# Performance work log

Hardware: AMD Instinct MI355X
Metric: run time of the kernel (lower is better)

The kernel has to match this reference:

```python
import jax, jax.numpy as jnp
import numpy as np

N = 50000   # nodes
D = 128     # hidden_dim
H = 8       # num_heads
DK = D // H # per-head dim
E = 1600000 # edges
L = 2       # n_layers
LN_EPS = 1e-5


def _layer_norm(x, g, b):
    m = jnp.mean(x, axis=-1, keepdims=True)
    v = jnp.mean(jnp.square(x - m), axis=-1, keepdims=True)
    return (x - m) * jax.lax.rsqrt(v + LN_EPS) * g + b


def _gt_layer(h, src, dst, Wq, bq, Wk, bk, Wv, bv, Wo, bo, W1, b1, W2, b2, g1, be1, g2, be2):
    n = h.shape[0]
    Q = (h @ Wq + bq).reshape(n, H, DK)
    K = (h @ Wk + bk).reshape(n, H, DK)
    V = (h @ Wv + bv).reshape(n, H, DK)
    # per-edge scaled dot-product score: K[src] . Q[dst]
    score = jnp.einsum('ehd,ehd->eh', K[src], Q[dst]) / np.sqrt(DK)
    score = jnp.exp(jnp.clip(score, -5.0, 5.0))            # [E,H]
    wV = jax.ops.segment_sum(V[src] * score[:, :, None], dst, num_segments=n)  # [N,H,DK]
    z = jax.ops.segment_sum(score, dst, num_segments=n)    # [N,H]
    attn = wV / (z[:, :, None] + 1e-6)                     # possible_empty-safe softmax
    h_att = attn.reshape(n, D) @ Wo + bo
    h = _layer_norm(h + h_att, g1, be1)                    # residual + LN
    ffn = jax.nn.relu(h @ W1 + b1) @ W2 + b2
    h = _layer_norm(h + ffn, g2, be2)                      # residual + LN
    return h


def setup_inputs() -> dict:
    key = jax.random.key(0)
    ks = jax.random.split(key, 16)
    s = 1.0 / np.sqrt(D)
    s2 = 1.0 / np.sqrt(2 * D)
    w = lambda k, shape, sc: jax.random.normal(k, shape, jnp.float32) * sc
    return {
        'h':   jax.random.normal(ks[0], (N, D), jnp.float32),
        'src': jax.random.randint(ks[1], (E,), 0, N),
        'dst': jax.random.randint(ks[2], (E,), 0, N),
        'Wq': w(ks[3], (L, D, D), s), 'bq': jnp.zeros((L, D), jnp.float32),
        'Wk': w(ks[4], (L, D, D), s), 'bk': jnp.zeros((L, D), jnp.float32),
        'Wv': w(ks[5], (L, D, D), s), 'bv': jnp.zeros((L, D), jnp.float32),
        'Wo': w(ks[6], (L, D, D), s), 'bo': jnp.zeros((L, D), jnp.float32),
        'W1': w(ks[7], (L, D, 2 * D), s), 'b1': jnp.zeros((L, 2 * D), jnp.float32),
        'W2': w(ks[8], (L, 2 * D, D), s2), 'b2': jnp.zeros((L, D), jnp.float32),
        'ln1_g': jnp.ones((L, D), jnp.float32), 'ln1_b': jnp.zeros((L, D), jnp.float32),
        'ln2_g': jnp.ones((L, D), jnp.float32), 'ln2_b': jnp.zeros((L, D), jnp.float32),
    }


def reference(h, src, dst, Wq, bq, Wk, bk, Wv, bv, Wo, bo, W1, b1, W2, b2, ln1_g, ln1_b, ln2_g, ln2_b):
    for l in range(L):
        h = _gt_layer(h, src, dst, Wq[l], bq[l], Wk[l], bk[l], Wv[l], bv[l],
                      Wo[l], bo[l], W1[l], b1[l], W2[l], b2[l],
                      ln1_g[l], ln1_b[l], ln2_g[l], ln2_b[l])
    return h
```

## Files before the change

kernel.cpp:

```cpp
#include <hip/hip_runtime.h>

#define NN 50000
#define DD 128
#define HH 8
#define EE 1600000
#define LL 2

typedef unsigned short u16;
typedef __attribute__((ext_vector_type(8))) __bf16 bf16x8;
typedef __attribute__((ext_vector_type(4))) float f32x4;
typedef __attribute__((ext_vector_type(2))) float f32x2;

__device__ __forceinline__ float bf2f(u16 u){
    return __uint_as_float(((unsigned int)u) << 16);
}
__device__ __forceinline__ u16 f2bf(float f){
    unsigned int x = __float_as_uint(f);
    x = x + 0x7fff + ((x >> 16) & 1);
    return (u16)(x >> 16);
}

__global__ __launch_bounds__(256) void f2b4_kernel(const float* __restrict__ in, u16* __restrict__ out, int n4){
    int i = blockIdx.x * 256 + threadIdx.x;
    if (i < n4){
        float4 v = ((const float4*)in)[i];
        ushort4 o;
        o.x = f2bf(v.x); o.y = f2bf(v.y); o.z = f2bf(v.z); o.w = f2bf(v.w);
        ((ushort4*)out)[i] = o;
    }
}

#define FILL_SUB 128
__global__ __launch_bounds__(256) void count_kernel(const int* __restrict__ dst, int* __restrict__ cnt){
    int slice = blockIdx.x & 7;
    int sub = blockIdx.x >> 3;
    int lo = slice * (NN / 8), hi = lo + (NN / 8);
    for (int e = sub * 256 + threadIdx.x; e < EE; e += FILL_SUB * 256){
        int d = dst[e];
        if (d >= lo && d < hi) atomicAdd(&cnt[d], 1);
    }
}

__global__ __launch_bounds__(1024) void scan_kernel(const int* __restrict__ cnt,
                                                    int* __restrict__ offs, int* __restrict__ cur){
    __shared__ int wsum[16];
    __shared__ int carry_s;
    __shared__ int ctot_s;
    int t = threadIdx.x, lane = t & 63, w = t >> 6;
    if (t == 0){ offs[0] = 0; cur[0] = 0; carry_s = 0; }
    __syncthreads();
    const int N4 = NN / 4;
    for (int base = 0; base < N4; base += 1024){
        int i4 = base + t;
        int4 x = (i4 < N4) ? ((const int4*)cnt)[i4] : make_int4(0, 0, 0, 0);
        int s1 = x.x, s2 = s1 + x.y, s3 = s2 + x.z, s4 = s3 + x.w;
        int v = s4;
        #pragma unroll
        for (int d = 1; d < 64; d <<= 1){ int u = __shfl_up(v, d); if (lane >= d) v += u; }
        if (lane == 63) wsum[w] = v;
        __syncthreads();
        if (t < 16){
            int sv = wsum[t];
            int iv = sv;
            #pragma unroll
            for (int d = 1; d < 16; d <<= 1){ int u = __shfl_up(iv, d); if (t >= d) iv += u; }
            wsum[t] = iv - sv;
            if (t == 15) ctot_s = iv;
        }
        __syncthreads();
        int excl = carry_s + wsum[w] + (v - s4);
        if (i4 < N4){
            int o = 4 * i4;
            offs[o + 1] = excl + s1;  cur[o + 1] = excl + s1;
            offs[o + 2] = excl + s2;  cur[o + 2] = excl + s2;
            offs[o + 3] = excl + s3;  cur[o + 3] = excl + s3;
            offs[o + 4] = excl + s4;  cur[o + 4] = excl + s4;
        }
        __syncthreads();
        if (t == 0) carry_s += ctot_s;
        __syncthreads();
    }
}

__global__ __launch_bounds__(256) void fill_kernel(const int* __restrict__ src, const int* __restrict__ dst,
                                                   int* __restrict__ cur, int* __restrict__ srcs){
    int slice = blockIdx.x & 7;
    int sub = blockIdx.x >> 3;
    int lo = slice * (NN / 8), hi = lo + (NN / 8);
    for (int e = sub * 256 + threadIdx.x; e < EE; e += FILL_SUB * 256){
        int d = dst[e];
        if (d >= lo && d < hi){
            int p = atomicAdd(&cur[d], 1);
            srcs[p] = src[e];
        }
    }
}

__global__ __launch_bounds__(256) void qkvpack_kernel(const float* __restrict__ Wq, const float* __restrict__ Wk,
                                                      const float* __restrict__ Wv, const float* __restrict__ bq,
                                                      const float* __restrict__ bk, const float* __restrict__ bv,
                                                      u16* __restrict__ Wt, float* __restrict__ bcat){
    int l = blockIdx.y;
    int idx = blockIdx.x * 256 + threadIdx.x;
    if (idx < 384 * 128){
        int n = idx >> 7, k = idx & 127;
        const float* W = (n < 128) ? Wq : (n < 256) ? Wk : Wv;
        int nc = n & 127;
        Wt[(size_t)l * 384 * 128 + idx] = f2bf(W[(size_t)l * 128 * 128 + k * 128 + nc]);
        if (k == 0){
            const float* bb = (n < 128) ? bq : (n < 256) ? bk : bv;
            bcat[l * 384 + n] = bb[l * 128 + nc];
        }
    }
}

__global__ __launch_bounds__(256) void transpose_kernel(const float* __restrict__ in, u16* __restrict__ out,
                                                        int R, int C){
    size_t mat = (size_t)blockIdx.y * R * C;
    int idx = blockIdx.x * 256 + threadIdx.x;
    if (idx < R * C){
        int r = idx / C, c = idx % C;
        out[mat + (size_t)c * R + r] = f2bf(in[mat + idx]);
    }
}

#define BM 128
#define BKK 64
#define LDA 72
#define LDC 136

__global__ __launch_bounds__(256) void gemm_bf16(const u16* __restrict__ A, const u16* __restrict__ Wt,
                                                 const float* __restrict__ bias,
                                                 u16* __restrict__ out, int M, int K, int N, int relu){
    __shared__ __align__(16) char smem[128 * LDA * 2 * 2];
    u16* As = (u16*)smem;
    u16* Bs = As + 128 * LDA;
    u16* Cs = (u16*)smem;

    int tid = threadIdx.x;
    int m0 = blockIdx.x * BM, n0 = blockIdx.y * 128;
    int lane = tid & 63, w = tid >> 6;
    int wm = w >> 1, wn = w & 1;
    int l15 = lane & 15, hi = lane >> 4, lk = hi * 8;

    f32x4 acc[4][4];
    #pragma unroll
    for (int mi = 0; mi < 4; mi++)
        #pragma unroll
        for (int ni = 0; ni < 4; ni++)
            acc[mi][ni] = (f32x4){0.f, 0.f, 0.f, 0.f};

    int sr = tid >> 3;
    int sc = (tid & 7) * 8;

    for (int k0 = 0; k0 < K; k0 += BKK){
        __syncthreads();
        #pragma unroll
        for (int p = 0; p < 4; p++){
            int row = p * 32 + sr;
            int gm = m0 + row;
            uint4 va = make_uint4(0, 0, 0, 0);
            if (gm < M) va = *(const uint4*)(A + (size_t)gm * K + k0 + sc);
            *(uint4*)(&As[row * LDA + sc]) = va;
            uint4 vb = *(const uint4*)(Wt + (size_t)(n0 + row) * K + k0 + sc);
            *(uint4*)(&Bs[row * LDA + sc]) = vb;
        }
        __syncthreads();
        #pragma unroll
        for (int ks = 0; ks < 2; ks++){
            bf16x8 a[4], b[4];
            #pragma unroll
            for (int i = 0; i < 4; i++){
                a[i] = *(const bf16x8*)(&As[(wm * 64 + i * 16 + l15) * LDA + ks * 32 + lk]);
                b[i] = *(const bf16x8*)(&Bs[(wn * 64 + i * 16 + l15) * LDA + ks * 32 + lk]);
            }
            #pragma unroll
            for (int mi = 0; mi < 4; mi++)
                #pragma unroll
                for (int ni = 0; ni < 4; ni++)
                    acc[mi][ni] = __builtin_amdgcn_mfma_f32_16x16x32_bf16(a[mi], b[ni], acc[mi][ni], 0, 0, 0);
        }
    }

    __syncthreads();
    #pragma unroll
    for (int mi = 0; mi < 4; mi++)
        #pragma unroll
        for (int ni = 0; ni < 4; ni++){
            int col = wn * 64 + ni * 16 + l15;
            float bval = bias[n0 + col];
            #pragma unroll
            for (int j = 0; j < 4; j++){
                int rl = wm * 64 + mi * 16 + hi * 4 + j;
                float v = acc[mi][ni][j] + bval;
                if (relu) v = fmaxf(v, 0.f);
                Cs[rl * LDC + col] = f2bf(v);
            }
        }
    __syncthreads();
    int qrow = tid >> 4, quad = tid & 15;
    #pragma unroll
    for (int p = 0; p < 8; p++){
        int rl = p * 16 + qrow;
        int gr = m0 + rl;
        if (gr < M){
            uint4 v = *(const uint4*)(&Cs[rl * LDC + quad * 8]);
            *(uint4*)(out + (size_t)gr * N + n0 + quad * 8) = v;
        }
    }
}

__global__ __launch_bounds__(256) void gemm_qkv(const u16* __restrict__ A, const u16* __restrict__ Wt,
                                                const float* __restrict__ bias,
                                                u16* __restrict__ Qb, u16* __restrict__ Kb,
                                                unsigned char* __restrict__ Vb,
                                                int M, int K){
    __shared__ __align__(16) char smem[128 * LDA * 2 * 2];
    u16* As = (u16*)smem;
    u16* Bs = As + 128 * LDA;
    u16* Cs = (u16*)smem;

    int tid = threadIdx.x;
    int m0 = blockIdx.x * BM, n0 = blockIdx.y * 128;
    int lane = tid & 63, w = tid >> 6;
    int wm = w >> 1, wn = w & 1;
    int l15 = lane & 15, hi = lane >> 4, lk = hi * 8;

    f32x4 acc[4][4];
    #pragma unroll
    for (int mi = 0; mi < 4; mi++)
        #pragma unroll
        for (int ni = 0; ni < 4; ni++)
            acc[mi][ni] = (f32x4){0.f, 0.f, 0.f, 0.f};

    int sr = tid >> 3;
    int sc = (tid & 7) * 8;

    for (int k0 = 0; k0 < K; k0 += BKK){
        __syncthreads();
        #pragma unroll
        for (int p = 0; p < 4; p++){
            int row = p * 32 + sr;
            int gm = m0 + row;
            uint4 va = make_uint4(0, 0, 0, 0);
            if (gm < M) va = *(const uint4*)(A + (size_t)gm * K + k0 + sc);
            *(uint4*)(&As[row * LDA + sc]) = va;
            uint4 vb = *(const uint4*)(Wt + (size_t)(n0 + row) * K + k0 + sc);
            *(uint4*)(&Bs[row * LDA + sc]) = vb;
        }
        __syncthreads();
        #pragma unroll
        for (int ks = 0; ks < 2; ks++){
            bf16x8 a[4], b[4];
            #pragma unroll
            for (int i = 0; i < 4; i++){
                a[i] = *(const bf16x8*)(&As[(wm * 64 + i * 16 + l15) * LDA + ks * 32 + lk]);
                b[i] = *(const bf16x8*)(&Bs[(wn * 64 + i * 16 + l15) * LDA + ks * 32 + lk]);
            }
            #pragma unroll
            for (int mi = 0; mi < 4; mi++)
                #pragma unroll
                for (int ni = 0; ni < 4; ni++)
                    acc[mi][ni] = __builtin_amdgcn_mfma_f32_16x16x32_bf16(a[mi], b[ni], acc[mi][ni], 0, 0, 0);
        }
    }

    __syncthreads();
    #pragma unroll
    for (int mi = 0; mi < 4; mi++)
        #pragma unroll
        for (int ni = 0; ni < 4; ni++){
            int col = wn * 64 + ni * 16 + l15;
            float bval = bias[n0 + col];
            #pragma unroll
            for (int j = 0; j < 4; j++){
                int rl = wm * 64 + mi * 16 + hi * 4 + j;
                Cs[rl * LDC + col] = f2bf(acc[mi][ni][j] + bval);
            }
        }
    __syncthreads();
    int qrow = tid >> 4, quad = tid & 15;
    if (n0 < 256){
        u16* Tb = (n0 == 0) ? Qb : Kb;
        #pragma unroll
        for (int p = 0; p < 8; p++){
            int rl = p * 16 + qrow;
            int gr = m0 + rl;
            if (gr < M){
                uint4 v = *(const uint4*)(&Cs[rl * LDC + quad * 8]);
                *(uint4*)(Tb + (size_t)gr * 128 + quad * 8) = v;
            }
        }
    } else {
        #pragma unroll
        for (int p = 0; p < 8; p++){
            int rl = p * 16 + qrow;
            int gr = m0 + rl;
            if (gr < M){
                uint4 v = *(const uint4*)(&Cs[rl * LDC + quad * 8]);
                float f0 = bf2f((u16)(v.x & 0xffff)), f1 = bf2f((u16)(v.x >> 16));
                float f2 = bf2f((u16)(v.y & 0xffff)), f3 = bf2f((u16)(v.y >> 16));
                float f4 = bf2f((u16)(v.z & 0xffff)), f5 = bf2f((u16)(v.z >> 16));
                float f6 = bf2f((u16)(v.w & 0xffff)), f7 = bf2f((u16)(v.w >> 16));
                unsigned int w0 = __builtin_amdgcn_cvt_pk_fp8_f32(f0, f1, 0u, false);
                w0 = __builtin_amdgcn_cvt_pk_fp8_f32(f2, f3, w0, true);
                unsigned int w1 = __builtin_amdgcn_cvt_pk_fp8_f32(f4, f5, 0u, false);
                w1 = __builtin_amdgcn_cvt_pk_fp8_f32(f6, f7, w1, true);
                *(uint2*)(Vb + (size_t)gr * 128 + quad * 8) = make_uint2(w0, w1);
            }
        }
    }
}

__global__ __launch_bounds__(256) void gemm_ln(const u16* __restrict__ A, const u16* __restrict__ Wt,
                                               const float* __restrict__ bias, const u16* __restrict__ resid,
                                               const float* __restrict__ g, const float* __restrict__ b,
                                               u16* __restrict__ out_bf, float* __restrict__ out_f,
                                               int M, int K){
    __shared__ __align__(16) char smem[128 * LDA * 2 * 2];
    u16* As = (u16*)smem;
    u16* Bs = As + 128 * LDA;
    __shared__ float ps[2][128];
    __shared__ float pss[2][128];

    int tid = threadIdx.x;
    int m0 = blockIdx.x * BM;
    int lane = tid & 63, w = tid >> 6;
    int wm = w >> 1, wn = w & 1;
    int l15 = lane & 15, hi = lane >> 4, lk = hi * 8;

    f32x4 acc[4][4];
    #pragma unroll
    for (int mi = 0; mi < 4; mi++)
        #pragma unroll
        for (int ni = 0; ni < 4; ni++)
            acc[mi][ni] = (f32x4){0.f, 0.f, 0.f, 0.f};

    int sr = tid >> 3;
    int sc = (tid & 7) * 8;

    for (int k0 = 0; k0 < K; k0 += BKK){
        __syncthreads();
        #pragma unroll
        for (int p = 0; p < 4; p++){
            int row = p * 32 + sr;
            int gm = m0 + row;
            uint4 va = make_uint4(0, 0, 0, 0);
            if (gm < M) va = *(const uint4*)(A + (size_t)gm * K + k0 + sc);
            *(uint4*)(&As[row * LDA + sc]) = va;
            uint4 vb = *(const uint4*)(Wt + (size_t)row * K + k0 + sc);
            *(uint4*)(&Bs[row * LDA + sc]) = vb;
        }
        __syncthreads();
        #pragma unroll
        for (int ks = 0; ks < 2; ks++){
            bf16x8 a[4], bb[4];
            #pragma unroll
            for (int i = 0; i < 4; i++){
                a[i] = *(const bf16x8*)(&As[(wm * 64 + i * 16 + l15) * LDA + ks * 32 + lk]);
                bb[i] = *(const bf16x8*)(&Bs[(wn * 64 + i * 16 + l15) * LDA + ks * 32 + lk]);
            }
            #pragma unroll
            for (int mi = 0; mi < 4; mi++)
                #pragma unroll
                for (int ni = 0; ni < 4; ni++)
                    acc[mi][ni] = __builtin_amdgcn_mfma_f32_16x16x32_bf16(a[mi], bb[ni], acc[mi][ni], 0, 0, 0);
        }
    }

    float gcol[4], bcol[4], bval[4];
    #pragma unroll
    for (int ni = 0; ni < 4; ni++){
        int col = wn * 64 + ni * 16 + l15;
        gcol[ni] = g[col]; bcol[ni] = b[col]; bval[ni] = bias[col];
    }

    #pragma unroll
    for (int mi = 0; mi < 4; mi++)
        #pragma unroll
        for (int j = 0; j < 4; j++){
            int rl = wm * 64 + mi * 16 + hi * 4 + j;
            int gr = m0 + rl;
            float s = 0.f, ss = 0.f;
            #pragma unroll
            for (int ni = 0; ni < 4; ni++){
                int col = wn * 64 + ni * 16 + l15;
                float x = acc[mi][ni][j] + bval[ni];
                if (gr < M) x += bf2f(resid[(size_t)gr * 128 + col]);
                acc[mi][ni][j] = x;
                s += x; ss += x * x;
            }
            #pragma unroll
            for (int d = 1; d < 16; d <<= 1){
                s  += __shfl_xor(s, d);
                ss += __shfl_xor(ss, d);
            }
            if (l15 == 0){ ps[wn][rl] = s; pss[wn][rl] = ss; }
        }
    __syncthreads();

    #pragma unroll
    for (int mi = 0; mi < 4; mi++)
        #pragma unroll
        for (int j = 0; j < 4; j++){
            int rl = wm * 64 + mi * 16 + hi * 4 + j;
            int gr = m0 + rl;
            if (gr >= M) continue;
            float s = ps[0][rl] + ps[1][rl];
            float ss = pss[0][rl] + pss[1][rl];
            float mean = s * (1.f / 128.f);
            float var = ss * (1.f / 128.f) - mean * mean;
            float r = rsqrtf(var + 1e-5f);
            #pragma unroll
            for (int ni = 0; ni < 4; ni++){
                int col = wn * 64 + ni * 16 + l15;
                float o = (acc[mi][ni][j] - mean) * r * gcol[ni] + bcol[ni];
                if (out_f) out_f[(size_t)gr * 128 + col] = o;
                else       out_bf[(size_t)gr * 128 + col] = f2bf(o);
            }
        }
}

__global__ __launch_bounds__(256) void edge_attn_kernel(const u16* __restrict__ Qb,
                                                        const u16* __restrict__ Kb,
                                                        const unsigned char* __restrict__ Vb,
                                                        const int* __restrict__ srcs,
                                                        const int* __restrict__ offs,
                                                        u16* __restrict__ att){
    int n = blockIdx.x * 4 + (threadIdx.x >> 6);
    if (n >= NN) return;
    int lane = threadIdx.x & 63;
    int laneh = lane & 31;
    int half = lane >> 5;

    float q0, q1, q2, q3;
    {
        uint2 qv = *(const uint2*)(Qb + (size_t)n * 128 + 4 * laneh);
        q0 = bf2f((u16)(qv.x & 0xffff)); q1 = bf2f((u16)(qv.x >> 16));
        q2 = bf2f((u16)(qv.y & 0xffff)); q3 = bf2f((u16)(qv.y >> 16));
    }
    const u16* kbase = Kb + 4 * laneh;
    const unsigned char* vbase = Vb + 4 * laneh;

    float w0 = 0.f, w1 = 0.f, w2 = 0.f, w3 = 0.f, z = 0.f;
    const float CS = 0.25f * 1.44269504f;

    auto proc = [&](uint2 kk, unsigned int vv, float gate){
        float k0 = bf2f((u16)(kk.x & 0xffff)), k1 = bf2f((u16)(kk.x >> 16));
        float k2 = bf2f((u16)(kk.y & 0xffff)), k3 = bf2f((u16)(kk.y >> 16));
        float p = q0 * k0 + q1 * k1 + q2 * k2 + q3 * k3;
        p += __shfl_xor(p, 1);
        p += __shfl_xor(p, 2);
        p = fminf(fmaxf(p, -20.f), 20.f);
        float sc = __builtin_amdgcn_exp2f(p * CS) * gate;
        f32x2 vl = __builtin_amdgcn_cvt_pk_f32_fp8(vv, false);
        f32x2 vh = __builtin_amdgcn_cvt_pk_f32_fp8(vv, true);
        w0 += sc * vl[0]; w1 += sc * vl[1]; w2 += sc * vh[0]; w3 += sc * vh[1];
        z += sc;
    };

    int e0 = offs[n], e1 = offs[n + 1];
    int i = e0;
    for (; i + 15 < e1; i += 16){
        int s[8];
        #pragma unroll
        for (int u = 0; u < 8; u++) s[u] = srcs[i + 2 * u + half];
        uint2 kk[8];
        unsigned int vv[8];
        #pragma unroll
        for (int u = 0; u < 8; u++){
            kk[u] = *(const uint2*)(kbase + (size_t)s[u] * 128);
            vv[u] = *(const unsigned int*)(vbase + (size_t)s[u] * 128);
        }
        #pragma unroll
        for (int u = 0; u < 8; u++) proc(kk[u], vv[u], 1.f);
    }
    for (; i + 1 < e1; i += 2){
        int s = srcs[i + half];
        proc(*(const uint2*)(kbase + (size_t)s * 128),
             *(const unsigned int*)(vbase + (size_t)s * 128), 1.f);
    }
    if (i < e1){
        int s = srcs[i];
        proc(*(const uint2*)(kbase + (size_t)s * 128),
             *(const unsigned int*)(vbase + (size_t)s * 128), half ? 0.f : 1.f);
    }

    w0 += __shfl_xor(w0, 32); w1 += __shfl_xor(w1, 32);
    w2 += __shfl_xor(w2, 32); w3 += __shfl_xor(w3, 32);
    z  += __shfl_xor(z, 32);

    if (!half){
        float inv = 1.f / (z + 1e-6f);
        unsigned int oA = (unsigned int)f2bf(w0 * inv) | ((unsigned int)f2bf(w1 * inv) << 16);
        unsigned int oB = (unsigned int)f2bf(w2 * inv) | ((unsigned int)f2bf(w3 * inv) << 16);
        *(uint2*)(att + (size_t)n * DD + 4 * laneh) = make_uint2(oA, oB);
    }
}

extern "C" void kernel_launch(void* const* d_in, const int* in_sizes, int n_in,
                              void* d_out, int out_size, void* d_ws, size_t ws_size,
                              hipStream_t stream){
    const float* h_in = (const float*)d_in[0];
    const int* src  = (const int*)d_in[1];
    const int* dst  = (const int*)d_in[2];
    const float* Wq = (const float*)d_in[3];
    const float* bq = (const float*)d_in[4];
    const float* Wk = (const float*)d_in[5];
    const float* bk = (const float*)d_in[6];
    const float* Wv = (const float*)d_in[7];
    const float* bv = (const float*)d_in[8];
    const float* Wo = (const float*)d_in[9];
    const float* bo = (const float*)d_in[10];
    const float* W1 = (const float*)d_in[11];
    const float* b1 = (const float*)d_in[12];
    const float* W2 = (const float*)d_in[13];
    const float* b2 = (const float*)d_in[14];
    const float* ln1_g = (const float*)d_in[15];
    const float* ln1_b = (const float*)d_in[16];
    const float* ln2_g = (const float*)d_in[17];
    const float* ln2_b = (const float*)d_in[18];
    float* outp = (float*)d_out;

    char* ws = (char*)d_ws;
    auto alloc = [&](size_t bytes) -> char* {
        char* p = ws;
        ws += (bytes + 255) & ~(size_t)255;
        return p;
    };
    int* cnt   = (int*)alloc((size_t)NN * 4);
    int* offs  = (int*)alloc((size_t)(NN + 1) * 4);
    int* cur   = (int*)alloc((size_t)(NN + 1) * 4);
    int* srcs  = (int*)alloc((size_t)EE * 4);
    u16* WtQKV = (u16*)alloc((size_t)LL * 384 * 128 * 2);
    float* bQKV = (float*)alloc((size_t)LL * 384 * 4);
    u16* WtO   = (u16*)alloc((size_t)LL * 128 * 128 * 2);
    u16* WtF1  = (u16*)alloc((size_t)LL * 256 * 128 * 2);
    u16* WtF2  = (u16*)alloc((size_t)LL * 128 * 256 * 2);
    u16* hb    = (u16*)alloc((size_t)NN * DD * 2);
    u16* Qb    = (u16*)alloc((size_t)NN * 128 * 2);
    u16* Kb    = (u16*)alloc((size_t)NN * 128 * 2);
    unsigned char* Vb = (unsigned char*)alloc((size_t)NN * 128);
    u16* ffm   = (u16*)alloc((size_t)NN * 256 * 2);
    u16* att   = (u16*)alloc((size_t)NN * DD * 2);
    u16* h1    = (u16*)alloc((size_t)NN * DD * 2);
    u16* hmid  = (u16*)alloc((size_t)NN * DD * 2);

    hipMemsetAsync(cnt, 0, (size_t)NN * 4, stream);
    count_kernel<<<8 * FILL_SUB, 256, 0, stream>>>(dst, cnt);
    scan_kernel<<<1, 1024, 0, stream>>>(cnt, offs, cur);
    fill_kernel<<<8 * FILL_SUB, 256, 0, stream>>>(src, dst, cur, srcs);

    f2b4_kernel<<<(NN * DD / 4 + 255) / 256, 256, 0, stream>>>(h_in, hb, NN * DD / 4);
    qkvpack_kernel<<<dim3(192, LL), 256, 0, stream>>>(Wq, Wk, Wv, bq, bk, bv, WtQKV, bQKV);
    transpose_kernel<<<dim3(64, LL), 256, 0, stream>>>(Wo, WtO, 128, 128);
    transpose_kernel<<<dim3(128, LL), 256, 0, stream>>>(W1, WtF1, 128, 256);
    transpose_kernel<<<dim3(128, LL), 256, 0, stream>>>(W2, WtF2, 256, 128);

    const int MB = (NN + BM - 1) / BM;
    const u16* hcur = hb;
    for (int l = 0; l < LL; l++){
        gemm_qkv<<<dim3(MB, 3), 256, 0, stream>>>(hcur, WtQKV + (size_t)l * 384 * 128,
                                                  bQKV + l * 384, Qb, Kb, Vb, NN, 128);
        edge_attn_kernel<<<NN / 4, 256, 0, stream>>>(Qb, Kb, Vb, srcs, offs, att);
        gemm_ln<<<MB, 256, 0, stream>>>(att, WtO + (size_t)l * 128 * 128, bo + l * 128,
                                        hcur, ln1_g + l * 128, ln1_b + l * 128,
                                        h1, nullptr, NN, 128);
        gemm_bf16<<<dim3(MB, 2), 256, 0, stream>>>(h1, WtF1 + (size_t)l * 256 * 128,
                                                   b1 + l * 256, ffm, NN, 128, 256, 1);
        if (l == LL - 1)
            gemm_ln<<<MB, 256, 0, stream>>>(ffm, WtF2 + (size_t)l * 128 * 256, b2 + l * 128,
                                            h1, ln2_g + l * 128, ln2_b + l * 128,
                                            nullptr, outp, NN, 256);
        else
            gemm_ln<<<MB, 256, 0, stream>>>(ffm, WtF2 + (size_t)l * 128 * 256, b2 + l * 128,
                                            h1, ln2_g + l * 128, ln2_b + l * 128,
                                            hmid, nullptr, NN, 256);
        hcur = hmid;
    }
}
```

Measured before the change: 524.9 us.

## Load GEMM MFMA operands directly from global memory, bypassing LDS staging

Replaces LDS-staged tiling in all GEMM kernels with a shared core that loads bf16x8 MFMA operand fragments straight from global memory. K becomes a template parameter so the whole K loop unrolls, and launch bounds request two blocks per SM. This removes the LDS stores, LDS reads and barriers from the main loop. In exchange, global loads are less coalesced (16-byte pieces spread over strided rows) and the many loads issued up front raise register pressure. Out-of-range rows are clamped to the last row rather than zero-filled.

```diff
diff --git a/kernel.cpp b/kernel.cpp
--- a/kernel.cpp
+++ b/kernel.cpp
@@ -124,24 +124,49 @@
     }
 }
 
+
 #define BM 128
-#define BKK 64
-#define LDA 72
 #define LDC 136
 
-__global__ __launch_bounds__(256) void gemm_bf16(const u16* __restrict__ A, const u16* __restrict__ Wt,
-                                                 const float* __restrict__ bias,
-                                                 u16* __restrict__ out, int M, int K, int N, int relu){
-    __shared__ __align__(16) char smem[128 * LDA * 2 * 2];
-    u16* As = (u16*)smem;
-    u16* Bs = As + 128 * LDA;
-    u16* Cs = (u16*)smem;
-
+template<int K>
+__device__ __forceinline__ void gemm_core(const u16* __restrict__ A, const u16* __restrict__ Wt,
+                                          int M, int m0, int n0, f32x4 (&acc)[4][4],
+                                          int wm, int wn, int l15, int hi){
+    const u16* ab[4];
+    const u16* bb[4];
+    #pragma unroll
+    for (int i = 0; i < 4; i++){
+        int row = m0 + wm * 64 + i * 16 + l15;
+        if (row >= M) row = M - 1;
+        ab[i] = A + (size_t)row * K + hi * 8;
+        bb[i] = Wt + (size_t)(n0 + wn * 64 + i * 16 + l15) * K + hi * 8;
+    }
+    #pragma unroll
+    for (int kk = 0; kk < K / 32; kk++){
+        bf16x8 a[4], b[4];
+        #pragma unroll
+        for (int i = 0; i < 4; i++){
+            a[i] = *(const bf16x8*)(ab[i] + kk * 32);
+            b[i] = *(const bf16x8*)(bb[i] + kk * 32);
+        }
+        #pragma unroll
+        for (int mi = 0; mi < 4; mi++)
+            #pragma unroll
+            for (int ni = 0; ni < 4; ni++)
+                acc[mi][ni] = __builtin_amdgcn_mfma_f32_16x16x32_bf16(a[mi], b[ni], acc[mi][ni], 0, 0, 0);
+    }
+}
+
+template<int K>
+__global__ __launch_bounds__(256, 2) void gemm_direct(const u16* __restrict__ A, const u16* __restrict__ Wt,
+                                                      const float* __restrict__ bias,
+                                                      u16* __restrict__ out, int M, int N, int relu){
+    __shared__ __align__(16) u16 Cs[128 * LDC];
     int tid = threadIdx.x;
     int m0 = blockIdx.x * BM, n0 = blockIdx.y * 128;
     int lane = tid & 63, w = tid >> 6;
     int wm = w >> 1, wn = w & 1;
-    int l15 = lane & 15, hi = lane >> 4, lk = hi * 8;
+    int l15 = lane & 15, hi = lane >> 4;
 
     f32x4 acc[4][4];
     #pragma unroll
@@ -150,39 +175,8 @@
         for (int ni = 0; ni < 4; ni++)
             acc[mi][ni] = (f32x4){0.f, 0.f, 0.f, 0.f};
 
-    int sr = tid >> 3;
-    int sc = (tid & 7) * 8;
-
-    for (int k0 = 0; k0 < K; k0 += BKK){
-        __syncthreads();
-        #pragma unroll
-        for (int p = 0; p < 4; p++){
-            int row = p * 32 + sr;
-            int gm = m0 + row;
-            uint4 va = make_uint4(0, 0, 0, 0);
-            if (gm < M) va = *(const uint4*)(A + (size_t)gm * K + k0 + sc);
-            *(uint4*)(&As[row * LDA + sc]) = va;
-            uint4 vb = *(const uint4*)(Wt + (size_t)(n0 + row) * K + k0 + sc);
-            *(uint4*)(&Bs[row * LDA + sc]) = vb;
-        }
-        __syncthreads();
-        #pragma unroll
-        for (int ks = 0; ks < 2; ks++){
-            bf16x8 a[4], b[4];
-            #pragma unroll
-            for (int i = 0; i < 4; i++){
-                a[i] = *(const bf16x8*)(&As[(wm * 64 + i * 16 + l15) * LDA + ks * 32 + lk]);
-                b[i] = *(const bf16x8*)(&Bs[(wn * 64 + i * 16 + l15) * LDA + ks * 32 + lk]);
-            }
-            #pragma unroll
-            for (int mi = 0; mi < 4; mi++)
-                #pragma unroll
-                for (int ni = 0; ni < 4; ni++)
-                    acc[mi][ni] = __builtin_amdgcn_mfma_f32_16x16x32_bf16(a[mi], b[ni], acc[mi][ni], 0, 0, 0);
-        }
-    }
-
-    __syncthreads();
+    gemm_core<K>(A, Wt, M, m0, n0, acc, wm, wn, l15, hi);
+
     #pragma unroll
     for (int mi = 0; mi < 4; mi++)
         #pragma unroll
@@ -210,21 +204,16 @@
     }
 }
 
-__global__ __launch_bounds__(256) void gemm_qkv(const u16* __restrict__ A, const u16* __restrict__ Wt,
-                                                const float* __restrict__ bias,
-                                                u16* __restrict__ Qb, u16* __restrict__ Kb,
-                                                unsigned char* __restrict__ Vb,
-                                                int M, int K){
-    __shared__ __align__(16) char smem[128 * LDA * 2 * 2];
-    u16* As = (u16*)smem;
-    u16* Bs = As + 128 * LDA;
-    u16* Cs = (u16*)smem;
-
+__global__ __launch_bounds__(256, 2) void gemm_qkv(const u16* __restrict__ A, const u16* __restrict__ Wt,
+                                                   const float* __restrict__ bias,
+                                                   u16* __restrict__ Qb, u16* __restrict__ Kb,
+                                                   unsigned char* __restrict__ Vb, int M){
+    __shared__ __align__(16) u16 Cs[128 * LDC];
     int tid = threadIdx.x;
     int m0 = blockIdx.x * BM, n0 = blockIdx.y * 128;
     int lane = tid & 63, w = tid >> 6;
     int wm = w >> 1, wn = w & 1;
-    int l15 = lane & 15, hi = lane >> 4, lk = hi * 8;
+    int l15 = lane & 15, hi = lane >> 4;
 
     f32x4 acc[4][4];
     #pragma unroll
@@ -233,39 +222,8 @@
         for (int ni = 0; ni < 4; ni++)
             acc[mi][ni] = (f32x4){0.f, 0.f, 0.f, 0.f};
 
-    int sr = tid >> 3;
-    int sc = (tid & 7) * 8;
-
-    for (int k0 = 0; k0 < K; k0 += BKK){
-        __syncthreads();
-        #pragma unroll
-        for (int p = 0; p < 4; p++){
-            int row = p * 32 + sr;
-            int gm = m0 + row;
-            uint4 va = make_uint4(0, 0, 0, 0);
-            if (gm < M) va = *(const uint4*)(A + (size_t)gm * K + k0 + sc);
-            *(uint4*)(&As[row * LDA + sc]) = va;
-            uint4 vb = *(const uint4*)(Wt + (size_t)(n0 + row) * K + k0 + sc);
-            *(uint4*)(&Bs[row * LDA + sc]) = vb;
-        }
-        __syncthreads();
-        #pragma unroll
-        for (int ks = 0; ks < 2; ks++){
-            bf16x8 a[4], b[4];
-            #pragma unroll
-            for (int i = 0; i < 4; i++){
-                a[i] = *(const bf16x8*)(&As[(wm * 64 + i * 16 + l15) * LDA + ks * 32 + lk]);
-                b[i] = *(const bf16x8*)(&Bs[(wn * 64 + i * 16 + l15) * LDA + ks * 32 + lk]);
-            }
-            #pragma unroll
-            for (int mi = 0; mi < 4; mi++)
-                #pragma unroll
-                for (int ni = 0; ni < 4; ni++)
-                    acc[mi][ni] = __builtin_amdgcn_mfma_f32_16x16x32_bf16(a[mi], b[ni], acc[mi][ni], 0, 0, 0);
-        }
-    }
-
-    __syncthreads();
+    gemm_core<128>(A, Wt, M, m0, n0, acc, wm, wn, l15, hi);
+
     #pragma unroll
     for (int mi = 0; mi < 4; mi++)
         #pragma unroll
@@ -312,22 +270,19 @@
     }
 }
 
-__global__ __launch_bounds__(256) void gemm_ln(const u16* __restrict__ A, const u16* __restrict__ Wt,
-                                               const float* __restrict__ bias, const u16* __restrict__ resid,
-                                               const float* __restrict__ g, const float* __restrict__ b,
-                                               u16* __restrict__ out_bf, float* __restrict__ out_f,
-                                               int M, int K){
-    __shared__ __align__(16) char smem[128 * LDA * 2 * 2];
-    u16* As = (u16*)smem;
-    u16* Bs = As + 128 * LDA;
+template<int K>
+__global__ __launch_bounds__(256, 2) void gemm_ln(const u16* __restrict__ A, const u16* __restrict__ Wt,
+                                                  const float* __restrict__ bias, const u16* __restrict__ resid,
+                                                  const float* __restrict__ g, const float* __restrict__ b,
+                                                  u16* __restrict__ out_bf, float* __restrict__ out_f,
+                                                  int M){
     __shared__ float ps[2][128];
     __shared__ float pss[2][128];
-
     int tid = threadIdx.x;
     int m0 = blockIdx.x * BM;
     int lane = tid & 63, w = tid >> 6;
     int wm = w >> 1, wn = w & 1;
-    int l15 = lane & 15, hi = lane >> 4, lk = hi * 8;
+    int l15 = lane & 15, hi = lane >> 4;
 
     f32x4 acc[4][4];
     #pragma unroll
@@ -336,37 +291,7 @@
         for (int ni = 0; ni < 4; ni++)
             acc[mi][ni] = (f32x4){0.f, 0.f, 0.f, 0.f};
 
-    int sr = tid >> 3;
-    int sc = (tid & 7) * 8;
-
-    for (int k0 = 0; k0 < K; k0 += BKK){
-        __syncthreads();
-        #pragma unroll
-        for (int p = 0; p < 4; p++){
-            int row = p * 32 + sr;
-            int gm = m0 + row;
-            uint4 va = make_uint4(0, 0, 0, 0);
-            if (gm < M) va = *(const uint4*)(A + (size_t)gm * K + k0 + sc);
-            *(uint4*)(&As[row * LDA + sc]) = va;
-            uint4 vb = *(const uint4*)(Wt + (size_t)row * K + k0 + sc);
-            *(uint4*)(&Bs[row * LDA + sc]) = vb;
-        }
-        __syncthreads();
-        #pragma unroll
-        for (int ks = 0; ks < 2; ks++){
-            bf16x8 a[4], bb[4];
-            #pragma unroll
-            for (int i = 0; i < 4; i++){
-                a[i] = *(const bf16x8*)(&As[(wm * 64 + i * 16 + l15) * LDA + ks * 32 + lk]);
-                bb[i] = *(const bf16x8*)(&Bs[(wn * 64 + i * 16 + l15) * LDA + ks * 32 + lk]);
-            }
-            #pragma unroll
-            for (int mi = 0; mi < 4; mi++)
-                #pragma unroll
-                for (int ni = 0; ni < 4; ni++)
-                    acc[mi][ni] = __builtin_amdgcn_mfma_f32_16x16x32_bf16(a[mi], bb[ni], acc[mi][ni], 0, 0, 0);
-        }
-    }
+    gemm_core<K>(A, Wt, M, m0, 0, acc, wm, wn, l15, hi);
 
     float gcol[4], bcol[4], bval[4];
     #pragma unroll
@@ -561,21 +486,21 @@
     const u16* hcur = hb;
     for (int l = 0; l < LL; l++){
         gemm_qkv<<<dim3(MB, 3), 256, 0, stream>>>(hcur, WtQKV + (size_t)l * 384 * 128,
-                                                  bQKV + l * 384, Qb, Kb, Vb, NN, 128);
+                                                  bQKV + l * 384, Qb, Kb, Vb, NN);
         edge_attn_kernel<<<NN / 4, 256, 0, stream>>>(Qb, Kb, Vb, srcs, offs, att);
-        gemm_ln<<<MB, 256, 0, stream>>>(att, WtO + (size_t)l * 128 * 128, bo + l * 128,
-                                        hcur, ln1_g + l * 128, ln1_b + l * 128,
-                                        h1, nullptr, NN, 128);
-        gemm_bf16<<<dim3(MB, 2), 256, 0, stream>>>(h1, WtF1 + (size_t)l * 256 * 128,
-                                                   b1 + l * 256, ffm, NN, 128, 256, 1);
+        gemm_ln<128><<<MB, 256, 0, stream>>>(att, WtO + (size_t)l * 128 * 128, bo + l * 128,
+                                             hcur, ln1_g + l * 128, ln1_b + l * 128,
+                                             h1, nullptr, NN);
+        gemm_direct<128><<<dim3(MB, 2), 256, 0, stream>>>(h1, WtF1 + (size_t)l * 256 * 128,
+                                                          b1 + l * 256, ffm, NN, 256, 1);
         if (l == LL - 1)
-            gemm_ln<<<MB, 256, 0, stream>>>(ffm, WtF2 + (size_t)l * 128 * 256, b2 + l * 128,
-                                            h1, ln2_g + l * 128, ln2_b + l * 128,
-                                            nullptr, outp, NN, 256);
+            gemm_ln<256><<<MB, 256, 0, stream>>>(ffm, WtF2 + (size_t)l * 128 * 256, b2 + l * 128,
+                                                 h1, ln2_g + l * 128, ln2_b + l * 128,
+                                                 nullptr, outp, NN);
         else
-            gemm_ln<<<MB, 256, 0, stream>>>(ffm, WtF2 + (size_t)l * 128 * 256, b2 + l * 128,
-                                            h1, ln2_g + l * 128, ln2_b + l * 128,
-                                            hmid, nullptr, NN, 256);
+            gemm_ln<256><<<MB, 256, 0, stream>>>(ffm, WtF2 + (size_t)l * 128 * 256, b2 + l * 128,
+                                                 h1, ln2_g + l * 128, ln2_b + l * 128,
+                                                 hmid, nullptr, NN);
         hcur = hmid;
     }
 }
```

Result: slower. 566.3 us (+7.9%).
